# Kernel tuning notes

Measured on AMD Instinct MI355X. Metric: run time of the kernel, lower is better.

## Reference

```python
import jax, jax.numpy as jnp
import numpy as np

EMBED_DIM = 768
NUM_HEADS = 12
HEAD_DIM = EMBED_DIM // NUM_HEADS
B, T = 2, 2048


def setup_inputs() -> dict:
    key = jax.random.key(0)
    ks = jax.random.split(key, 11)
    s = 1.0 / np.sqrt(EMBED_DIM)
    return {
        "query": jax.random.normal(ks[0], (B, T, EMBED_DIM), jnp.float32),
        "key_in": jax.random.normal(ks[1], (B, T, EMBED_DIM), jnp.float32),
        "value": jax.random.normal(ks[2], (B, T, EMBED_DIM), jnp.float32),
        "Wq": jax.random.uniform(ks[3], (EMBED_DIM, EMBED_DIM), jnp.float32, -s, s),
        "bq": jnp.zeros((EMBED_DIM,), jnp.float32),
        "Wk": jax.random.uniform(ks[4], (EMBED_DIM, EMBED_DIM), jnp.float32, -s, s),
        "bk": jnp.zeros((EMBED_DIM,), jnp.float32),
        "Wv": jax.random.uniform(ks[5], (EMBED_DIM, EMBED_DIM), jnp.float32, -s, s),
        "bv": jnp.zeros((EMBED_DIM,), jnp.float32),
        "Wo": jax.random.uniform(ks[6], (EMBED_DIM, EMBED_DIM), jnp.float32, -s, s),
        "bo": jnp.zeros((EMBED_DIM,), jnp.float32),
    }


def reference(query, key_in, value, Wq, bq, Wk, bk, Wv, bv, Wo, bo):
    b, t, _ = query.shape

    def split_heads(x):  # [B,T,E] -> [B,H,T,Dh]
        return x.reshape(b, t, NUM_HEADS, HEAD_DIM).transpose(0, 2, 1, 3)

    Q = split_heads(query @ Wq + bq)
    K = split_heads(key_in @ Wk + bk)
    V = split_heads(value @ Wv + bv)

    scores = jnp.einsum("bhqd,bhkd->bhqk", Q, K) / np.sqrt(HEAD_DIM).astype(np.float32)
    attn = jax.nn.softmax(scores, axis=-1)
    out = jnp.einsum("bhqk,bhkd->bhqd", attn, V)  # [B,H,T,Dh]
    out = out.transpose(0, 2, 1, 3).reshape(b, t, EMBED_DIM)
    return out @ Wo + bo
```

## Files before the change

### kernel.cpp

```cpp
#include <hip/hip_runtime.h>
#include <math.h>

typedef __attribute__((ext_vector_type(4))) float  floatx4;
typedef __attribute__((ext_vector_type(8))) short  short8;
typedef __attribute__((ext_vector_type(4))) short  short4v;
typedef __attribute__((ext_vector_type(8))) __bf16 bf16x8;

#define E_DIM 768
#define T_DIM 2048
#define N_B   2
#define N_H   12
#define H_D   64
#define M_TOT 4096

#define Q_SCALE 0.1803368801111204f

#if __has_builtin(__builtin_amdgcn_exp2f)
#define EXP2F(x) __builtin_amdgcn_exp2f(x)
#else
#define EXP2F(x) exp2f(x)
#endif
#if __has_builtin(__builtin_amdgcn_rcpf)
#define RCPF(x) __builtin_amdgcn_rcpf(x)
#else
#define RCPF(x) (1.0f / (x))
#endif

__device__ __forceinline__ unsigned short f32_to_bf16(float f) {
  unsigned int u = __float_as_uint(f);
  u += 0x7fffu + ((u >> 16) & 1u);
  return (unsigned short)(u >> 16);
}

__device__ __forceinline__ unsigned short f32_to_bf16_trunc(float f) {
  return (unsigned short)(__float_as_uint(f) >> 16);
}

__device__ __forceinline__ void lds_barrier() {
  asm volatile("s_waitcnt lgkmcnt(0)\n\ts_barrier" ::: "memory");
}

__device__ __forceinline__ void gload_lds16(const unsigned short* g, unsigned short* l) {
  __builtin_amdgcn_global_load_lds(
      (const __attribute__((address_space(1))) unsigned int*)(const void*)g,
      (__attribute__((address_space(3))) unsigned int*)(void*)l, 16, 0, 0);
}

__global__ __launch_bounds__(256) void convert_x(const float* __restrict__ q,
                                                 const float* __restrict__ k,
                                                 const float* __restrict__ v,
                                                 unsigned short* __restrict__ Xb) {
  const int z = blockIdx.y;
  const float* src = (z == 0) ? q : (z == 1) ? k : v;
  size_t idx = ((size_t)blockIdx.x * 256 + threadIdx.x) * 4;
  float4 val = *reinterpret_cast<const float4*>(&src[idx]);
  short4v o;
  o[0] = (short)f32_to_bf16(val.x);
  o[1] = (short)f32_to_bf16(val.y);
  o[2] = (short)f32_to_bf16(val.z);
  o[3] = (short)f32_to_bf16(val.w);
  *reinterpret_cast<short4v*>(&Xb[(size_t)z * M_TOT * E_DIM + idx]) = o;
}

__global__ __launch_bounds__(256) void transpose_w4(const float* __restrict__ W0,
                                                    const float* __restrict__ W1,
                                                    const float* __restrict__ W2,
                                                    const float* __restrict__ W3,
                                                    unsigned short* __restrict__ Wt) {
  __shared__ float tile[32][33];
  const int z = blockIdx.z;
  const float* W = (z == 0) ? W0 : (z == 1) ? W1 : (z == 2) ? W2 : W3;
  unsigned short* dst = Wt + (size_t)z * E_DIM * E_DIM;
  int k0 = blockIdx.x * 32, n0 = blockIdx.y * 32;
  int tx = threadIdx.x & 31, ty = threadIdx.x >> 5;
  for (int i = 0; i < 4; i++)
    tile[ty + i * 8][tx] = W[(size_t)(k0 + ty + i * 8) * E_DIM + n0 + tx];
  __syncthreads();
  for (int i = 0; i < 4; i++)
    dst[(size_t)(n0 + ty + i * 8) * E_DIM + k0 + tx] = f32_to_bf16(tile[tx][ty + i * 8]);
}

__global__ __launch_bounds__(256) void gemm_qkv(const unsigned short* __restrict__ Xb,
                                                const unsigned short* __restrict__ WtAll,
                                                const float* __restrict__ bq,
                                                const float* __restrict__ bk,
                                                const float* __restrict__ bv,
                                                unsigned short* __restrict__ outQKV) {
  __shared__ unsigned short As[128 * 32];
  __shared__ unsigned short Bs[128 * 32];

  const int z = blockIdx.z;
  const unsigned short* A = Xb + (size_t)z * M_TOT * E_DIM;
  const float* bias = (z == 0) ? bq : (z == 1) ? bk : bv;
  const unsigned short* W = WtAll + (size_t)z * E_DIM * E_DIM;
  unsigned short* out = outQKV + (size_t)z * M_TOT * E_DIM;
  const float scale = (z == 0) ? Q_SCALE : 1.0f;

  const int tid = threadIdx.x;
  const int lane = tid & 63, wv = tid >> 6;
  const int m15 = lane & 15, quad = lane >> 4;
  const int wm = (wv & 1) * 64, wn = (wv >> 1) * 64;
  const int m0 = blockIdx.x * 128, n0 = blockIdx.y * 128;

  floatx4 acc[4][4] = {};
  const int srow = lane >> 2, scol = (lane & 3) * 8;

  for (int k0 = 0; k0 < E_DIM; k0 += 32) {
    for (int cc = 0; cc < 2; cc++) {
      int c = wv * 2 + cc;
      gload_lds16(&A[(size_t)(m0 + c * 16 + srow) * E_DIM + k0 + scol], &As[c * 512]);
      gload_lds16(&W[(size_t)(n0 + c * 16 + srow) * E_DIM + k0 + scol], &Bs[c * 512]);
    }
    __syncthreads();
    bf16x8 af[4], bfr[4];
    for (int i = 0; i < 4; i++)
      af[i] = *reinterpret_cast<const bf16x8*>(&As[(wm + i * 16 + m15) * 32 + quad * 8]);
    for (int j = 0; j < 4; j++)
      bfr[j] = *reinterpret_cast<const bf16x8*>(&Bs[(wn + j * 16 + m15) * 32 + quad * 8]);
    for (int i = 0; i < 4; i++)
      for (int j = 0; j < 4; j++)
        acc[i][j] = __builtin_amdgcn_mfma_f32_16x16x32_bf16(af[i], bfr[j], acc[i][j], 0, 0, 0);
    __syncthreads();
  }

  for (int i = 0; i < 4; i++)
    for (int j = 0; j < 4; j++) {
      int gn = n0 + wn + j * 16 + m15;
      int h = gn >> 6, d = gn & 63;
      float bso = bias[gn];
      for (int r = 0; r < 4; r++) {
        int gm = m0 + wm + i * 16 + quad * 4 + r;
        int bb = gm >> 11, tt = gm & 2047;
        float v = (acc[i][j][r] + bso) * scale;
        out[(((size_t)bb * N_H + h) * T_DIM + tt) * H_D + d] = f32_to_bf16(v);
      }
    }
}

__global__ __launch_bounds__(256) void transpose_v(const unsigned short* __restrict__ Vg_all,
                                                   unsigned short* __restrict__ VT) {
  __shared__ unsigned short tile[64 * 72];
  const int t0 = blockIdx.x * 64, h = blockIdx.y, bb = blockIdx.z;
  const unsigned short* Vg = Vg_all + (((size_t)bb * N_H + h) * T_DIM) * H_D;
  unsigned short* VTh = VT + (((size_t)bb * N_H + h) * H_D) * T_DIM;
  const int tid = threadIdx.x;
  const int tloc = tid & 63, d0 = (tid >> 6) * 16;

  short8 r0 = *reinterpret_cast<const short8*>(&Vg[(size_t)(t0 + tloc) * H_D + d0]);
  short8 r1 = *reinterpret_cast<const short8*>(&Vg[(size_t)(t0 + tloc) * H_D + d0 + 8]);
#pragma unroll
  for (int j = 0; j < 8; j++) {
    tile[(d0 + j) * 72 + tloc] = (unsigned short)r0[j];
    tile[(d0 + 8 + j) * 72 + tloc] = (unsigned short)r1[j];
  }
  __syncthreads();
  const int d = tid >> 2, ts = (tid & 3) * 16;
  short8 w0 = *reinterpret_cast<const short8*>(&tile[d * 72 + ts]);
  short8 w1 = *reinterpret_cast<const short8*>(&tile[d * 72 + ts + 8]);
  *reinterpret_cast<short8*>(&VTh[(size_t)d * T_DIM + t0 + ts]) = w0;
  *reinterpret_cast<short8*>(&VTh[(size_t)d * T_DIM + t0 + ts + 8]) = w1;
}

__global__ __launch_bounds__(256) void attn(const unsigned short* __restrict__ QKV,
                                            const unsigned short* __restrict__ VT,
                                            unsigned short* __restrict__ ctx) {
  __shared__ unsigned short Qs[64 * 72];
  __shared__ unsigned short Sb[64 * 72];
  __shared__ unsigned short Ks[64 * 72];
  __shared__ unsigned short Vs[2][64 * 72];

  const int qt = blockIdx.x, h = blockIdx.y, bb = blockIdx.z;
  const size_t headoff = (((size_t)bb * N_H + h) * T_DIM) * H_D;
  const unsigned short* Qg = QKV + headoff;
  const unsigned short* Kg = QKV + (size_t)M_TOT * E_DIM + headoff;
  const unsigned short* VTg = VT + (((size_t)bb * N_H + h) * H_D) * T_DIM;

  const int tid = threadIdx.x, lane = tid & 63, wv = tid >> 6;
  const int m15 = lane & 15, quad = lane >> 4;
  const int q0 = qt * 64;
  const int rs = tid >> 3, cs = (tid & 7) * 8;

  for (int p = 0; p < 2; p++)
    *reinterpret_cast<short8*>(&Qs[(p * 32 + rs) * 72 + cs]) =
        *reinterpret_cast<const short8*>(&Qg[(size_t)(q0 + p * 32 + rs) * H_D + cs]);

  short8 kreg[2], vreg[2];
  for (int p = 0; p < 2; p++) {
    kreg[p] = *reinterpret_cast<const short8*>(&Kg[(size_t)(p * 32 + rs) * H_D + cs]);
    vreg[p] = *reinterpret_cast<const short8*>(&VTg[(size_t)(p * 32 + rs) * T_DIM + cs]);
  }
  lds_barrier();

  bf16x8 aq[2];
  aq[0] = *reinterpret_cast<const bf16x8*>(&Qs[(wv * 16 + m15) * 72 + 0 + quad * 8]);
  aq[1] = *reinterpret_cast<const bf16x8*>(&Qs[(wv * 16 + m15) * 72 + 32 + quad * 8]);

  for (int p = 0; p < 2; p++) {
    *reinterpret_cast<short8*>(&Ks[(p * 32 + rs) * 72 + cs]) = kreg[p];
    *reinterpret_cast<short8*>(&Vs[0][(p * 32 + rs) * 72 + cs]) = vreg[p];
  }
  for (int p = 0; p < 2; p++) {
    kreg[p] = *reinterpret_cast<const short8*>(&Kg[(size_t)(64 + p * 32 + rs) * H_D + cs]);
    vreg[p] = *reinterpret_cast<const short8*>(&VTg[(size_t)(p * 32 + rs) * T_DIM + 64 + cs]);
  }
  lds_barrier();

  floatx4 o[4] = {};
  floatx4 lacc = {};
  const short8 ones_s = {0x3f80, 0x3f80, 0x3f80, 0x3f80, 0x3f80, 0x3f80, 0x3f80, 0x3f80};
  const bf16x8 onesb = __builtin_bit_cast(bf16x8, ones_s);
  unsigned short* stripA = &Qs[wv * 16 * 72];
  unsigned short* stripB = &Sb[wv * 16 * 72];

  {
    floatx4 s[4] = {};
    for (int kk = 0; kk < 2; kk++)
      for (int j = 0; j < 4; j++) {
        bf16x8 b = *reinterpret_cast<const bf16x8*>(&Ks[(j * 16 + m15) * 72 + kk * 32 + quad * 8]);
        s[j] = __builtin_amdgcn_mfma_f32_16x16x32_bf16(aq[kk], b, s[j], 0, 0, 0);
      }
    lds_barrier();
    for (int p = 0; p < 2; p++) {
      *reinterpret_cast<short8*>(&Ks[(p * 32 + rs) * 72 + cs]) = kreg[p];
      *reinterpret_cast<short8*>(&Vs[1][(p * 32 + rs) * 72 + cs]) = vreg[p];
    }
    for (int p = 0; p < 2; p++) {
      kreg[p] = *reinterpret_cast<const short8*>(&Kg[(size_t)(128 + p * 32 + rs) * H_D + cs]);
      vreg[p] = *reinterpret_cast<const short8*>(&VTg[(size_t)(p * 32 + rs) * T_DIM + 128 + cs]);
    }
    for (int j = 0; j < 4; j++)
      for (int r = 0; r < 4; r++)
        stripA[(quad * 4 + r) * 72 + j * 16 + m15] = f32_to_bf16_trunc(EXP2F(s[j][r]));
  }

  for (int kt = 1; kt < 32; kt++) {
    unsigned short* sp_prev = (kt & 1) ? stripA : stripB;
    unsigned short* sp_cur = (kt & 1) ? stripB : stripA;
    const unsigned short* vprev = Vs[(kt - 1) & 1];
    lds_barrier();

    for (int kk = 0; kk < 2; kk++) {
      bf16x8 a = *reinterpret_cast<const bf16x8*>(&sp_prev[m15 * 72 + kk * 32 + quad * 8]);
      lacc = __builtin_amdgcn_mfma_f32_16x16x32_bf16(a, onesb, lacc, 0, 0, 0);
      for (int j = 0; j < 4; j++) {
        bf16x8 b = *reinterpret_cast<const bf16x8*>(&vprev[(j * 16 + m15) * 72 + kk * 32 + quad * 8]);
        o[j] = __builtin_amdgcn_mfma_f32_16x16x32_bf16(a, b, o[j], 0, 0, 0);
      }
    }

    floatx4 s[4] = {};
    for (int kk = 0; kk < 2; kk++)
      for (int j = 0; j < 4; j++) {
        bf16x8 b = *reinterpret_cast<const bf16x8*>(&Ks[(j * 16 + m15) * 72 + kk * 32 + quad * 8]);
        s[j] = __builtin_amdgcn_mfma_f32_16x16x32_bf16(aq[kk], b, s[j], 0, 0, 0);
      }
    lds_barrier();

    if (kt < 31) {
      for (int p = 0; p < 2; p++) {
        *reinterpret_cast<short8*>(&Ks[(p * 32 + rs) * 72 + cs]) = kreg[p];
        *reinterpret_cast<short8*>(&Vs[(kt + 1) & 1][(p * 32 + rs) * 72 + cs]) = vreg[p];
      }
      if (kt < 30)
        for (int p = 0; p < 2; p++) {
          kreg[p] = *reinterpret_cast<const short8*>(&Kg[(size_t)((kt + 2) * 64 + p * 32 + rs) * H_D + cs]);
          vreg[p] = *reinterpret_cast<const short8*>(&VTg[(size_t)(p * 32 + rs) * T_DIM + (kt + 2) * 64 + cs]);
        }
    }

    for (int j = 0; j < 4; j++)
      for (int r = 0; r < 4; r++)
        sp_cur[(quad * 4 + r) * 72 + j * 16 + m15] = f32_to_bf16_trunc(EXP2F(s[j][r]));
  }

  asm volatile("s_waitcnt lgkmcnt(0)" ::: "memory");
  for (int kk = 0; kk < 2; kk++) {
    bf16x8 a = *reinterpret_cast<const bf16x8*>(&stripB[m15 * 72 + kk * 32 + quad * 8]);
    lacc = __builtin_amdgcn_mfma_f32_16x16x32_bf16(a, onesb, lacc, 0, 0, 0);
    for (int j = 0; j < 4; j++) {
      bf16x8 b = *reinterpret_cast<const bf16x8*>(&Vs[1][(j * 16 + m15) * 72 + kk * 32 + quad * 8]);
      o[j] = __builtin_amdgcn_mfma_f32_16x16x32_bf16(a, b, o[j], 0, 0, 0);
    }
  }

  for (int r = 0; r < 4; r++) {
    float rl = RCPF(lacc[r]);
    int q = q0 + wv * 16 + quad * 4 + r;
    for (int j = 0; j < 4; j++)
      ctx[(size_t)(bb * T_DIM + q) * E_DIM + h * 64 + j * 16 + m15] = f32_to_bf16(o[j][r] * rl);
  }
}

__global__ __launch_bounds__(256) void gemm_out(const unsigned short* __restrict__ Actx,
                                                const unsigned short* __restrict__ Wt,
                                                const float* __restrict__ bias,
                                                float* __restrict__ out) {
  __shared__ unsigned short As[64 * 32];
  __shared__ unsigned short Bs[128 * 32];

  const int tid = threadIdx.x;
  const int lane = tid & 63, wv = tid >> 6;
  const int m15 = lane & 15, quad = lane >> 4;
  const int wm = (wv & 1) * 32, wn = (wv >> 1) * 64;
  const int m0 = blockIdx.x * 64, n0 = blockIdx.y * 128;

  floatx4 acc[2][4] = {};
  const int srow = lane >> 2, scol = (lane & 3) * 8;

  for (int k0 = 0; k0 < E_DIM; k0 += 32) {
    gload_lds16(&Actx[(size_t)(m0 + wv * 16 + srow) * E_DIM + k0 + scol], &As[wv * 512]);
    for (int cc = 0; cc < 2; cc++) {
      int c = wv * 2 + cc;
      gload_lds16(&Wt[(size_t)(n0 + c * 16 + srow) * E_DIM + k0 + scol], &Bs[c * 512]);
    }
    __syncthreads();
    bf16x8 af[2], bfr[4];
    for (int i = 0; i < 2; i++)
      af[i] = *reinterpret_cast<const bf16x8*>(&As[(wm + i * 16 + m15) * 32 + quad * 8]);
    for (int j = 0; j < 4; j++)
      bfr[j] = *reinterpret_cast<const bf16x8*>(&Bs[(wn + j * 16 + m15) * 32 + quad * 8]);
    for (int i = 0; i < 2; i++)
      for (int j = 0; j < 4; j++)
        acc[i][j] = __builtin_amdgcn_mfma_f32_16x16x32_bf16(af[i], bfr[j], acc[i][j], 0, 0, 0);
    __syncthreads();
  }

  for (int i = 0; i < 2; i++)
    for (int j = 0; j < 4; j++) {
      int gn = n0 + wn + j * 16 + m15;
      float bso = bias[gn];
      for (int r = 0; r < 4; r++) {
        int gm = m0 + wm + i * 16 + quad * 4 + r;
        out[(size_t)gm * E_DIM + gn] = acc[i][j][r] + bso;
      }
    }
}

extern "C" void kernel_launch(void* const* d_in, const int* in_sizes, int n_in,
                              void* d_out, int out_size, void* d_ws, size_t ws_size,
                              hipStream_t stream) {
  const float* query  = (const float*)d_in[0];
  const float* key_in = (const float*)d_in[1];
  const float* value  = (const float*)d_in[2];
  const float* Wq = (const float*)d_in[3];
  const float* bq = (const float*)d_in[4];
  const float* Wk = (const float*)d_in[5];
  const float* bk = (const float*)d_in[6];
  const float* Wv = (const float*)d_in[7];
  const float* bv = (const float*)d_in[8];
  const float* Wo = (const float*)d_in[9];
  const float* bo = (const float*)d_in[10];
  float* out = (float*)d_out;

  unsigned short* ws  = (unsigned short*)d_ws;
  unsigned short* Wt  = ws;
  unsigned short* Xb  = Wt + (size_t)4 * E_DIM * E_DIM;
  unsigned short* QKV = Xb + (size_t)3 * M_TOT * E_DIM;
  unsigned short* VT  = QKV + (size_t)3 * M_TOT * E_DIM;
  unsigned short* ctx = VT + (size_t)N_B * N_H * H_D * T_DIM;

  dim3 tb(256);
  convert_x<<<dim3(M_TOT * E_DIM / 1024, 3), tb, 0, stream>>>(query, key_in, value, Xb);
  transpose_w4<<<dim3(24, 24, 4), tb, 0, stream>>>(Wq, Wk, Wv, Wo, Wt);

  gemm_qkv<<<dim3(32, 6, 3), tb, 0, stream>>>(Xb, Wt, bq, bk, bv, QKV);
  transpose_v<<<dim3(32, 12, 2), tb, 0, stream>>>(QKV + (size_t)2 * M_TOT * E_DIM, VT);
  attn<<<dim3(32, 12, 2), tb, 0, stream>>>(QKV, VT, ctx);
  gemm_out<<<dim3(64, 6), tb, 0, stream>>>(ctx, Wt + (size_t)3 * E_DIM * E_DIM, bo, out);
  (void)in_sizes; (void)n_in; (void)out_size; (void)ws_size;
}
```

Before: 202.7 us.

## Restructure attention into single-wave blocks loading K/V fragments directly to registers

The attention kernel now runs one wavefront per block, each handling 32 query rows (two 16-row groups). K and V^T MFMA operand fragments are loaded straight from global memory into double-buffered registers instead of being staged through shared LDS tiles, so block-wide barriers go away and each K/V fragment is reused across both query groups. The exp strip still goes through a small per-wave LDS buffer. In exchange, each wave issues uncoalesced strided global loads, every wave fetches K/V independently with no cross-wave sharing in LDS, and register pressure rises.

Result: slower. 239.4 us (+18.1%).

```diff
diff --git a/kernel.cpp b/kernel.cpp
--- a/kernel.cpp
+++ b/kernel.cpp
@@ -34,10 +34,6 @@
 
 __device__ __forceinline__ unsigned short f32_to_bf16_trunc(float f) {
   return (unsigned short)(__float_as_uint(f) >> 16);
-}
-
-__device__ __forceinline__ void lds_barrier() {
-  asm volatile("s_waitcnt lgkmcnt(0)\n\ts_barrier" ::: "memory");
 }
 
 __device__ __forceinline__ void gload_lds16(const unsigned short* g, unsigned short* l) {
@@ -161,134 +157,126 @@
   *reinterpret_cast<short8*>(&VTh[(size_t)d * T_DIM + t0 + ts + 8]) = w1;
 }
 
-__global__ __launch_bounds__(256) void attn(const unsigned short* __restrict__ QKV,
-                                            const unsigned short* __restrict__ VT,
-                                            unsigned short* __restrict__ ctx) {
-  __shared__ unsigned short Qs[64 * 72];
-  __shared__ unsigned short Sb[64 * 72];
-  __shared__ unsigned short Ks[64 * 72];
-  __shared__ unsigned short Vs[2][64 * 72];
-
-  const int qt = blockIdx.x, h = blockIdx.y, bb = blockIdx.z;
+__global__ __launch_bounds__(64) void attn(const unsigned short* __restrict__ QKV,
+                                           const unsigned short* __restrict__ VT,
+                                           unsigned short* __restrict__ ctx) {
+  __shared__ unsigned short strip[32 * 72];
+
+  const int qw = blockIdx.x, h = blockIdx.y, bb = blockIdx.z;
   const size_t headoff = (((size_t)bb * N_H + h) * T_DIM) * H_D;
   const unsigned short* Qg = QKV + headoff;
   const unsigned short* Kg = QKV + (size_t)M_TOT * E_DIM + headoff;
   const unsigned short* VTg = VT + (((size_t)bb * N_H + h) * H_D) * T_DIM;
 
-  const int tid = threadIdx.x, lane = tid & 63, wv = tid >> 6;
+  const int lane = threadIdx.x;
   const int m15 = lane & 15, quad = lane >> 4;
-  const int q0 = qt * 64;
-  const int rs = tid >> 3, cs = (tid & 7) * 8;
-
-  for (int p = 0; p < 2; p++)
-    *reinterpret_cast<short8*>(&Qs[(p * 32 + rs) * 72 + cs]) =
-        *reinterpret_cast<const short8*>(&Qg[(size_t)(q0 + p * 32 + rs) * H_D + cs]);
-
-  short8 kreg[2], vreg[2];
-  for (int p = 0; p < 2; p++) {
-    kreg[p] = *reinterpret_cast<const short8*>(&Kg[(size_t)(p * 32 + rs) * H_D + cs]);
-    vreg[p] = *reinterpret_cast<const short8*>(&VTg[(size_t)(p * 32 + rs) * T_DIM + cs]);
-  }
-  lds_barrier();
-
-  bf16x8 aq[2];
-  aq[0] = *reinterpret_cast<const bf16x8*>(&Qs[(wv * 16 + m15) * 72 + 0 + quad * 8]);
-  aq[1] = *reinterpret_cast<const bf16x8*>(&Qs[(wv * 16 + m15) * 72 + 32 + quad * 8]);
-
-  for (int p = 0; p < 2; p++) {
-    *reinterpret_cast<short8*>(&Ks[(p * 32 + rs) * 72 + cs]) = kreg[p];
-    *reinterpret_cast<short8*>(&Vs[0][(p * 32 + rs) * 72 + cs]) = vreg[p];
-  }
-  for (int p = 0; p < 2; p++) {
-    kreg[p] = *reinterpret_cast<const short8*>(&Kg[(size_t)(64 + p * 32 + rs) * H_D + cs]);
-    vreg[p] = *reinterpret_cast<const short8*>(&VTg[(size_t)(p * 32 + rs) * T_DIM + 64 + cs]);
-  }
-  lds_barrier();
-
-  floatx4 o[4] = {};
-  floatx4 lacc = {};
+  const int q0 = qw * 32;
+
+  const unsigned short* kbase = Kg + (size_t)(m15 * 64 + quad * 8);
+  const unsigned short* vbase = VTg + (size_t)(m15 * 2048 + quad * 8);
+
+#define KFRAG(kt, j, kk) \
+  (*reinterpret_cast<const short8*>(kbase + (size_t)(kt) * 4096 + (j) * 1024 + (kk) * 32))
+#define VFRAG(kt, j, kk) \
+  (*reinterpret_cast<const short8*>(vbase + (size_t)(j) * 32768 + (kt) * 64 + (kk) * 32))
+
+  bf16x8 aq[2][2];
+  for (int g = 0; g < 2; g++)
+    for (int kk = 0; kk < 2; kk++)
+      aq[g][kk] = __builtin_bit_cast(bf16x8, *reinterpret_cast<const short8*>(
+          &Qg[(size_t)(q0 + g * 16 + m15) * 64 + kk * 32 + quad * 8]));
+
+  short8 kf[2][8], vf[2][8];
+#pragma unroll
+  for (int j = 0; j < 4; j++)
+    for (int kk = 0; kk < 2; kk++) {
+      kf[0][j * 2 + kk] = KFRAG(0, j, kk);
+      vf[0][j * 2 + kk] = VFRAG(0, j, kk);
+    }
+#pragma unroll
+  for (int j = 0; j < 4; j++)
+    for (int kk = 0; kk < 2; kk++) {
+      kf[1][j * 2 + kk] = KFRAG(1, j, kk);
+      vf[1][j * 2 + kk] = VFRAG(1, j, kk);
+    }
+
+  floatx4 o[2][4] = {};
+  floatx4 lacc[2] = {};
   const short8 ones_s = {0x3f80, 0x3f80, 0x3f80, 0x3f80, 0x3f80, 0x3f80, 0x3f80, 0x3f80};
   const bf16x8 onesb = __builtin_bit_cast(bf16x8, ones_s);
-  unsigned short* stripA = &Qs[wv * 16 * 72];
-  unsigned short* stripB = &Sb[wv * 16 * 72];
-
-  {
+
+  for (int g = 0; g < 2; g++) {
     floatx4 s[4] = {};
     for (int kk = 0; kk < 2; kk++)
-      for (int j = 0; j < 4; j++) {
-        bf16x8 b = *reinterpret_cast<const bf16x8*>(&Ks[(j * 16 + m15) * 72 + kk * 32 + quad * 8]);
-        s[j] = __builtin_amdgcn_mfma_f32_16x16x32_bf16(aq[kk], b, s[j], 0, 0, 0);
-      }
-    lds_barrier();
-    for (int p = 0; p < 2; p++) {
-      *reinterpret_cast<short8*>(&Ks[(p * 32 + rs) * 72 + cs]) = kreg[p];
-      *reinterpret_cast<short8*>(&Vs[1][(p * 32 + rs) * 72 + cs]) = vreg[p];
-    }
-    for (int p = 0; p < 2; p++) {
-      kreg[p] = *reinterpret_cast<const short8*>(&Kg[(size_t)(128 + p * 32 + rs) * H_D + cs]);
-      vreg[p] = *reinterpret_cast<const short8*>(&VTg[(size_t)(p * 32 + rs) * T_DIM + 128 + cs]);
-    }
+      for (int j = 0; j < 4; j++)
+        s[j] = __builtin_amdgcn_mfma_f32_16x16x32_bf16(
+            aq[g][kk], __builtin_bit_cast(bf16x8, kf[0][j * 2 + kk]), s[j], 0, 0, 0);
     for (int j = 0; j < 4; j++)
       for (int r = 0; r < 4; r++)
-        stripA[(quad * 4 + r) * 72 + j * 16 + m15] = f32_to_bf16_trunc(EXP2F(s[j][r]));
-  }
-
+        strip[(g * 16 + quad * 4 + r) * 72 + j * 16 + m15] = f32_to_bf16_trunc(EXP2F(s[j][r]));
+  }
+#pragma unroll
+  for (int j = 0; j < 4; j++)
+    for (int kk = 0; kk < 2; kk++) kf[0][j * 2 + kk] = KFRAG(2, j, kk);
+  asm volatile("s_waitcnt lgkmcnt(0)" ::: "memory");
+
+#pragma unroll 2
   for (int kt = 1; kt < 32; kt++) {
-    unsigned short* sp_prev = (kt & 1) ? stripA : stripB;
-    unsigned short* sp_cur = (kt & 1) ? stripB : stripA;
-    const unsigned short* vprev = Vs[(kt - 1) & 1];
-    lds_barrier();
-
-    for (int kk = 0; kk < 2; kk++) {
-      bf16x8 a = *reinterpret_cast<const bf16x8*>(&sp_prev[m15 * 72 + kk * 32 + quad * 8]);
-      lacc = __builtin_amdgcn_mfma_f32_16x16x32_bf16(a, onesb, lacc, 0, 0, 0);
-      for (int j = 0; j < 4; j++) {
-        bf16x8 b = *reinterpret_cast<const bf16x8*>(&vprev[(j * 16 + m15) * 72 + kk * 32 + quad * 8]);
-        o[j] = __builtin_amdgcn_mfma_f32_16x16x32_bf16(a, b, o[j], 0, 0, 0);
-      }
-    }
-
-    floatx4 s[4] = {};
+    const int cp = kt & 1, pp = cp ^ 1;
+
+    for (int g = 0; g < 2; g++)
+      for (int kk = 0; kk < 2; kk++) {
+        bf16x8 a = *reinterpret_cast<const bf16x8*>(&strip[(g * 16 + m15) * 72 + kk * 32 + quad * 8]);
+        lacc[g] = __builtin_amdgcn_mfma_f32_16x16x32_bf16(a, onesb, lacc[g], 0, 0, 0);
+        for (int j = 0; j < 4; j++)
+          o[g][j] = __builtin_amdgcn_mfma_f32_16x16x32_bf16(
+              a, __builtin_bit_cast(bf16x8, vf[pp][j * 2 + kk]), o[g][j], 0, 0, 0);
+      }
+
+    floatx4 s0[4] = {}, s1[4] = {};
     for (int kk = 0; kk < 2; kk++)
       for (int j = 0; j < 4; j++) {
-        bf16x8 b = *reinterpret_cast<const bf16x8*>(&Ks[(j * 16 + m15) * 72 + kk * 32 + quad * 8]);
-        s[j] = __builtin_amdgcn_mfma_f32_16x16x32_bf16(aq[kk], b, s[j], 0, 0, 0);
-      }
-    lds_barrier();
-
-    if (kt < 31) {
-      for (int p = 0; p < 2; p++) {
-        *reinterpret_cast<short8*>(&Ks[(p * 32 + rs) * 72 + cs]) = kreg[p];
-        *reinterpret_cast<short8*>(&Vs[(kt + 1) & 1][(p * 32 + rs) * 72 + cs]) = vreg[p];
-      }
-      if (kt < 30)
-        for (int p = 0; p < 2; p++) {
-          kreg[p] = *reinterpret_cast<const short8*>(&Kg[(size_t)((kt + 2) * 64 + p * 32 + rs) * H_D + cs]);
-          vreg[p] = *reinterpret_cast<const short8*>(&VTg[(size_t)(p * 32 + rs) * T_DIM + (kt + 2) * 64 + cs]);
-        }
-    }
+        bf16x8 b = __builtin_bit_cast(bf16x8, kf[cp][j * 2 + kk]);
+        s0[j] = __builtin_amdgcn_mfma_f32_16x16x32_bf16(aq[0][kk], b, s0[j], 0, 0, 0);
+        s1[j] = __builtin_amdgcn_mfma_f32_16x16x32_bf16(aq[1][kk], b, s1[j], 0, 0, 0);
+      }
+
+    if (kt < 30)
+#pragma unroll
+      for (int j = 0; j < 4; j++)
+        for (int kk = 0; kk < 2; kk++) kf[cp][j * 2 + kk] = KFRAG(kt + 2, j, kk);
+    if (kt < 31)
+#pragma unroll
+      for (int j = 0; j < 4; j++)
+        for (int kk = 0; kk < 2; kk++) vf[pp][j * 2 + kk] = VFRAG(kt + 1, j, kk);
 
     for (int j = 0; j < 4; j++)
-      for (int r = 0; r < 4; r++)
-        sp_cur[(quad * 4 + r) * 72 + j * 16 + m15] = f32_to_bf16_trunc(EXP2F(s[j][r]));
-  }
-
-  asm volatile("s_waitcnt lgkmcnt(0)" ::: "memory");
-  for (int kk = 0; kk < 2; kk++) {
-    bf16x8 a = *reinterpret_cast<const bf16x8*>(&stripB[m15 * 72 + kk * 32 + quad * 8]);
-    lacc = __builtin_amdgcn_mfma_f32_16x16x32_bf16(a, onesb, lacc, 0, 0, 0);
-    for (int j = 0; j < 4; j++) {
-      bf16x8 b = *reinterpret_cast<const bf16x8*>(&Vs[1][(j * 16 + m15) * 72 + kk * 32 + quad * 8]);
-      o[j] = __builtin_amdgcn_mfma_f32_16x16x32_bf16(a, b, o[j], 0, 0, 0);
-    }
-  }
-
-  for (int r = 0; r < 4; r++) {
-    float rl = RCPF(lacc[r]);
-    int q = q0 + wv * 16 + quad * 4 + r;
-    for (int j = 0; j < 4; j++)
-      ctx[(size_t)(bb * T_DIM + q) * E_DIM + h * 64 + j * 16 + m15] = f32_to_bf16(o[j][r] * rl);
-  }
+      for (int r = 0; r < 4; r++) {
+        strip[(quad * 4 + r) * 72 + j * 16 + m15] = f32_to_bf16_trunc(EXP2F(s0[j][r]));
+        strip[(16 + quad * 4 + r) * 72 + j * 16 + m15] = f32_to_bf16_trunc(EXP2F(s1[j][r]));
+      }
+    asm volatile("s_waitcnt lgkmcnt(0)" ::: "memory");
+  }
+
+  for (int g = 0; g < 2; g++)
+    for (int kk = 0; kk < 2; kk++) {
+      bf16x8 a = *reinterpret_cast<const bf16x8*>(&strip[(g * 16 + m15) * 72 + kk * 32 + quad * 8]);
+      lacc[g] = __builtin_amdgcn_mfma_f32_16x16x32_bf16(a, onesb, lacc[g], 0, 0, 0);
+      for (int j = 0; j < 4; j++)
+        o[g][j] = __builtin_amdgcn_mfma_f32_16x16x32_bf16(
+            a, __builtin_bit_cast(bf16x8, vf[1][j * 2 + kk]), o[g][j], 0, 0, 0);
+    }
+
+  for (int g = 0; g < 2; g++)
+    for (int r = 0; r < 4; r++) {
+      float rl = RCPF(lacc[g][r]);
+      int q = q0 + g * 16 + quad * 4 + r;
+      for (int j = 0; j < 4; j++)
+        ctx[(size_t)(bb * T_DIM + q) * E_DIM + h * 64 + j * 16 + m15] =
+            f32_to_bf16(o[g][j][r] * rl);
+    }
+#undef KFRAG
+#undef VFRAG
 }
 
 __global__ __launch_bounds__(256) void gemm_out(const unsigned short* __restrict__ Actx,
@@ -365,7 +353,7 @@
 
   gemm_qkv<<<dim3(32, 6, 3), tb, 0, stream>>>(Xb, Wt, bq, bk, bv, QKV);
   transpose_v<<<dim3(32, 12, 2), tb, 0, stream>>>(QKV + (size_t)2 * M_TOT * E_DIM, VT);
-  attn<<<dim3(32, 12, 2), tb, 0, stream>>>(QKV, VT, ctx);
+  attn<<<dim3(64, 12, 2), dim3(64), 0, stream>>>(QKV, VT, ctx);
   gemm_out<<<dim3(64, 6), tb, 0, stream>>>(ctx, Wt + (size_t)3 * E_DIM * E_DIM, bo, out);
   (void)in_sizes; (void)n_in; (void)out_size; (void)ws_size;
 }
```
